# Performance work log

Measured on AMD Instinct MI355X. Metric: run time of the kernel, lower is better.

The kernel has to match this reference:

```python
import jax, jax.numpy as jnp
import numpy as np

D_MODEL = 1024
N_HEADS = 16
D_HEAD = 64
D_FF = 4096
WINDOW = 256
B, T = 2, 2048


def setup_inputs() -> dict:
    key = jax.random.key(0)
    ks = jax.random.split(key, 10)
    tot = N_HEADS * D_HEAD
    def w(k, shape):
        # approximate kaiming_normal_ fan_out init: std = sqrt(2/fan_out)
        fan_out = shape[0]
        return jax.random.normal(k, shape, jnp.float32) * np.sqrt(2.0 / fan_out)
    return {
        "x": jax.random.normal(ks[0], (B, T, D_MODEL), jnp.float32),
        "ln1_w": jnp.ones((D_MODEL,), jnp.float32),
        "qkv_w": w(ks[1], (3 * tot, D_MODEL)),
        "gate_w": w(ks[2], (tot, D_MODEL)),
        "out_w": w(ks[3], (D_MODEL, tot)),
        "ln2_w": jnp.ones((D_MODEL,), jnp.float32),
        "wg": w(ks[4], (D_FF, D_MODEL)),
        "wu": w(ks[5], (D_FF, D_MODEL)),
        "wo": w(ks[6], (D_MODEL, D_FF)),
    }


def _rmsnorm(x, w):
    return x * jax.lax.rsqrt(jnp.mean(x * x, axis=-1, keepdims=True) + 1e-6) * w


def _attention(x, qkv_w, gate_w, out_w):
    Bq, Tq, _ = x.shape
    tot = N_HEADS * D_HEAD
    qkv = x @ qkv_w.T  # [B,T,3*tot]
    q, k, v = jnp.split(qkv, 3, axis=-1)
    q = q.reshape(Bq, Tq, N_HEADS, D_HEAD).transpose(0, 2, 1, 3)
    k = k.reshape(Bq, Tq, N_HEADS, D_HEAD).transpose(0, 2, 1, 3)
    v = v.reshape(Bq, Tq, N_HEADS, D_HEAD).transpose(0, 2, 1, 3)
    scale = D_HEAD ** -0.5
    scores = jnp.einsum("bhqd,bhkd->bhqk", q, k) * scale
    pos = jnp.arange(Tq)
    dist = pos[:, None] - pos[None, :]
    allowed = (dist >= 0) & (dist < WINDOW)  # causal sliding window
    mask = jnp.where(allowed, 0.0, -jnp.inf).astype(scores.dtype)
    attn = jax.nn.softmax(scores + mask[None, None], axis=-1)
    out = jnp.einsum("bhqk,bhkd->bhqd", attn, v)
    out = out.transpose(0, 2, 1, 3).reshape(Bq, Tq, tot)
    gate = jax.nn.sigmoid(x @ gate_w.T)
    return (out * gate) @ out_w.T


def reference(x, ln1_w, qkv_w, gate_w, out_w, ln2_w, wg, wu, wo):
    x = x + _attention(_rmsnorm(x, ln1_w), qkv_w, gate_w, out_w)
    h = _rmsnorm(x, ln2_w)
    ffn = (jax.nn.silu(h @ wg.T) * (h @ wu.T)) @ wo.T
    return x + ffn
```

## Files before the change

### kernel.cpp

```cpp
#include <hip/hip_runtime.h>


#define DEV __device__ __forceinline__

using u16 = unsigned short;
typedef __attribute__((ext_vector_type(8))) short  short8;
typedef __attribute__((ext_vector_type(4))) float  floatx4;

DEV u16 f2bf(float f) {
  unsigned u = __builtin_bit_cast(unsigned, f);
  u += 0x7FFFu + ((u >> 16) & 1u);
  return (u16)(u >> 16);
}
DEV float bf2f(u16 h) {
  unsigned u = ((unsigned)h) << 16;
  return __builtin_bit_cast(float, u);
}
DEV floatx4 mfma16(short8 a, short8 b, floatx4 c) {
  return __builtin_amdgcn_mfma_f32_16x16x32_bf16(a, b, c, 0, 0, 0);
}
DEV void gload16(const u16* g, const char* lds_base_wave_uniform) {
  __builtin_amdgcn_global_load_lds(
      (const __attribute__((address_space(1))) void*)g,
      (__attribute__((address_space(3))) void*)lds_base_wave_uniform,
      16, 0, 0);
}
#define WAITVM(n) asm volatile("s_waitcnt vmcnt(" #n ")" ::: "memory")
DEV void blockbar() {
  asm volatile("" ::: "memory");
  __builtin_amdgcn_s_barrier();
  asm volatile("" ::: "memory");
}

__global__ __launch_bounds__(256) void cvt_all_k(
    const float* __restrict__ s0, const float* __restrict__ s1,
    const float* __restrict__ s2, const float* __restrict__ s3,
    const float* __restrict__ s4, const float* __restrict__ s5,
    u16* __restrict__ d0, u16* __restrict__ d1, u16* __restrict__ d2,
    u16* __restrict__ d3, u16* __restrict__ d4, u16* __restrict__ d5) {
  const int b = blockIdx.x;
  const float* in; u16* out; int base;
  if (b < 3072)       { in = s0; out = d0; base = 0; }
  else if (b < 4096)  { in = s1; out = d1; base = 3072; }
  else if (b < 5120)  { in = s2; out = d2; base = 4096; }
  else if (b < 9216)  { in = s3; out = d3; base = 5120; }
  else if (b < 13312) { in = s4; out = d4; base = 9216; }
  else                { in = s5; out = d5; base = 13312; }
  const size_t i = (size_t)(b - base) * 256 + threadIdx.x;
  const float4 v = ((const float4*)in)[i];
  ushort4 r;
  r.x = f2bf(v.x); r.y = f2bf(v.y); r.z = f2bf(v.z); r.w = f2bf(v.w);
  ((ushort4*)out)[i] = r;
}

__global__ __launch_bounds__(256) void rmsnorm_k(const float* __restrict__ x,
                                                 const float* __restrict__ wt,
                                                 u16* __restrict__ o) {
  __shared__ float red[4];
  const int row = blockIdx.x;
  const int tid = threadIdx.x;
  const float4 v = ((const float4*)(x + (size_t)row * 1024))[tid];
  float ss = v.x * v.x + v.y * v.y + v.z * v.z + v.w * v.w;
  ss += __shfl_xor(ss, 1, 64);
  ss += __shfl_xor(ss, 2, 64);
  ss += __shfl_xor(ss, 4, 64);
  ss += __shfl_xor(ss, 8, 64);
  ss += __shfl_xor(ss, 16, 64);
  ss += __shfl_xor(ss, 32, 64);
  if ((tid & 63) == 0) red[tid >> 6] = ss;
  __syncthreads();
  const float tot = red[0] + red[1] + red[2] + red[3];
  const float sc = rsqrtf(tot * (1.0f / 1024.0f) + 1e-6f);
  const float4 wv = ((const float4*)wt)[tid];
  ushort4 r;
  r.x = f2bf(v.x * sc * wv.x);
  r.y = f2bf(v.y * sc * wv.y);
  r.z = f2bf(v.z * sc * wv.z);
  r.w = f2bf(v.w * sc * wv.w);
  ((ushort4*)(o + (size_t)row * 1024))[tid] = r;
}

__global__ __launch_bounds__(256) void reduce4_k(const u16* __restrict__ part,
                                                 const float* __restrict__ x2,
                                                 float* __restrict__ out) {
  const size_t i = ((size_t)blockIdx.x * 256 + threadIdx.x) * 4;
  float4 r = *(const float4*)(x2 + i);
#pragma unroll
  for (int s = 0; s < 4; s++) {
    const ushort4 pv = *(const ushort4*)(part + (size_t)s * 4194304 + i);
    r.x += bf2f(pv.x); r.y += bf2f(pv.y); r.z += bf2f(pv.z); r.w += bf2f(pv.w);
  }
  *(float4*)(out + i) = r;
}

template <int CFG, int EPI>
__global__ __launch_bounds__(512, 2) void gemm8p(
    const u16* __restrict__ Ag, const u16* __restrict__ Bg, int N, int K,
    int ksz, u16* __restrict__ cb, float* __restrict__ cf,
    const u16* __restrict__ aux, const float* __restrict__ resid,
    u16* __restrict__ cb2) {
  constexpr int BM = (CFG == 0) ? 256 : 128;
  constexpr int WM = (CFG == 0) ? 128 : 64;
  constexpr int WN = (CFG == 0) ? 64 : 32;
  constexpr int NI = WM / 16;
  constexpr int NJ = WN / 16;
  constexpr int IH = (CFG == 0) ? NI / 2 : NI;
  constexpr int GB = BM * 64;
  constexpr int QI = (CFG == 0) ? 2 : 1;
  constexpr int BUFB = 4 * GB;
  __shared__ __align__(16) char lds[2 * BUFB];

  const int tid = threadIdx.x;
  const int w = tid >> 6, lane = tid & 63;
  const int wm = w >> 2, wn = w & 3;
  const int g = lane >> 4, r16 = lane & 15;
  const int gx = (g ^ ((r16 >> 1) & 3)) << 4;

  int bid = blockIdx.y * gridDim.x + blockIdx.x;
  const int cpx = (gridDim.x * gridDim.y) >> 3;
  bid = (bid & 7) * cpx + (bid >> 3);
  const int m0 = (bid / gridDim.x) * BM;
  const int n0 = (bid % gridDim.x) * BM;
  const int kbeg = blockIdx.z * ksz;

  floatx4 acc[NI][NJ];
#pragma unroll
  for (int i = 0; i < NI; i++)
#pragma unroll
    for (int j = 0; j < NJ; j++) acc[i][j] = (floatx4){0.f, 0.f, 0.f, 0.f};

  const int nt = ksz >> 6;

  const int kg_src = (lane & 3) ^ ((lane >> 3) & 3);
  auto stageG = [&](int G, int t) {
    if (t >= nt) return;
    const u16* Mat = (G < 2) ? Ag : Bg;
    const int b0 = (G < 2) ? m0 : n0;
    const int kc = kbeg + t * 64 + (G & 1) * 32 + kg_src * 8;
    const char* dst = lds + (t & 1) * BUFB + G * GB + w * 1024;
#pragma unroll
    for (int q = 0; q < QI; q++) {
      const int row = q * 128 + w * 16 + (lane >> 2);
      gload16(Mat + (size_t)(b0 + row) * K + kc, dst + q * 8192);
    }
  };

  auto rdA = [&](short8* af, int ks, int ihalf, const char* buf) {
#pragma unroll
    for (int i = 0; i < IH; i++) {
      const int arow = wm * WM + (ihalf * IH + i) * 16 + r16;
      af[i] = *(const short8*)(buf + ks * GB + arow * 64 + gx);
    }
  };
  auto rdB = [&](short8* bf_, int ks, const char* buf) {
#pragma unroll
    for (int j = 0; j < NJ; j++) {
      const int brow = wn * WN + j * 16 + r16;
      bf_[j] = *(const short8*)(buf + 2 * GB + ks * GB + brow * 64 + gx);
    }
  };
  auto mm = [&](short8* af, short8* bf_, int ihalf) {
    __builtin_amdgcn_s_setprio(1);
#pragma unroll
    for (int i = 0; i < IH; i++)
#pragma unroll
      for (int j = 0; j < NJ; j++)
        acc[ihalf * IH + i][j] = mfma16(af[i], bf_[j], acc[ihalf * IH + i][j]);
    __builtin_amdgcn_s_setprio(0);
  };

  stageG(0, 0); stageG(2, 0); stageG(1, 0); stageG(3, 0);

  for (int t = 0; t < nt; ++t) {
    const char* buf = lds + (t & 1) * BUFB;
    if constexpr (CFG == 0) {
      short8 af0[IH], af1[IH], bfv[NJ];
      WAITVM(4);
      blockbar();
      rdA(af0, 0, 0, buf); rdB(bfv, 0, buf);
      stageG(0, t + 1);
      rdA(af1, 0, 1, buf);
      mm(af0, bfv, 0);
      blockbar();
      stageG(2, t + 1);
      mm(af1, bfv, 1);
      if (t + 1 < nt) { WAITVM(4); } else { WAITVM(0); }
      blockbar();
      rdA(af0, 1, 0, buf); rdB(bfv, 1, buf);
      stageG(1, t + 1);
      rdA(af1, 1, 1, buf);
      mm(af0, bfv, 0);
      blockbar();
      stageG(3, t + 1);
      mm(af1, bfv, 1);
    } else {
      short8 af[IH], bfv[NJ];
      WAITVM(2);
      blockbar();
      rdA(af, 0, 0, buf); rdB(bfv, 0, buf);
      stageG(0, t + 1); stageG(2, t + 1);
      mm(af, bfv, 0);
      if (t + 1 < nt) { WAITVM(2); } else { WAITVM(0); }
      blockbar();
      rdA(af, 1, 0, buf); rdB(bfv, 1, buf);
      stageG(1, t + 1); stageG(3, t + 1);
      mm(af, bfv, 0);
    }
  }

#pragma unroll
  for (int i = 0; i < NI; i++) {
    const int row = m0 + wm * WM + i * 16 + g * 4;
#pragma unroll
    for (int j = 0; j < NJ; j++) {
      const int col = n0 + wn * WN + j * 16 + r16;
#pragma unroll
      for (int rr = 0; rr < 4; rr++) {
        const float v = acc[i][j][rr];
        if constexpr (EPI == 2) {
          cb[(size_t)(row + rr) * N + col] = f2bf(v / (1.0f + __expf(-v)));
        } else if constexpr (EPI == 3) {
          const size_t idx = (size_t)(row + rr) * N + col;
          cb[idx] = f2bf(v * bf2f(aux[idx]));
        } else if constexpr (EPI == 4) {
          const size_t idx = (size_t)(row + rr) * N + col;
          cf[idx] = v + resid[idx];
        } else if constexpr (EPI == 6) {
          if (col < 3072)
            cb[(size_t)(row + rr) * 3072 + col] = f2bf(v);
          else
            cb2[(size_t)(row + rr) * 1024 + (col - 3072)] =
                f2bf(1.0f / (1.0f + __expf(-v)));
        } else if constexpr (EPI == 7) {
          (cb + (size_t)blockIdx.z * 4194304)[(size_t)(row + rr) * N + col] =
              f2bf(v);
        }
      }
    }
  }
}

__global__ __launch_bounds__(256) void attn_win_kernel(
    const u16* __restrict__ qkv, const u16* __restrict__ gate,
    u16* __restrict__ out) {
  __shared__ __align__(16) u16 Kl[64][80];
  __shared__ __align__(16) u16 Vt[64][80];
  __shared__ __align__(16) u16 Pl[4][16][80];

  const int tid = threadIdx.x;
  const int w = tid >> 6, lane = tid & 63;
  const int g = lane >> 4, r16 = lane & 15;

  const int q0 = blockIdx.x * 64;
  const int h = blockIdx.y;
  const int b = blockIdx.z;
  const u16* qb_ = qkv + (size_t)b * 2048 * 3072;

  const int tq = q0 + w * 16 + r16;
  const u16* qptr = qb_ + (size_t)tq * 3072 + h * 64;
  const short8 aq0 = *(const short8*)(qptr + g * 8);
  const short8 aq1 = *(const short8*)(qptr + 32 + g * 8);

  floatx4 O[4] = {{0,0,0,0},{0,0,0,0},{0,0,0,0},{0,0,0,0}};
  float mrow[4] = {-1e30f, -1e30f, -1e30f, -1e30f};
  float lrow[4] = {0.f, 0.f, 0.f, 0.f};

  const int srow = tid >> 2;
  const int sq4 = tid & 3;
  const int qw = q0 + w * 16;

  for (int kt = q0 - 256; kt <= q0; kt += 64) {
    if (kt < 0) continue;
    {
      const u16* kb = qb_ + (size_t)(kt + srow) * 3072 + 1024 + h * 64 + sq4 * 16;
      const short8 kv0 = *(const short8*)kb;
      const short8 kv1 = *(const short8*)(kb + 8);
      *(short8*)&Kl[srow][sq4 * 16] = kv0;
      *(short8*)&Kl[srow][sq4 * 16 + 8] = kv1;
      const u16* vb = kb + 1024;
      const short8 vv0 = *(const short8*)vb;
      const short8 vv1 = *(const short8*)(vb + 8);
#pragma unroll
      for (int j = 0; j < 8; j++) Vt[sq4 * 16 + j][srow] = (u16)vv0[j];
#pragma unroll
      for (int j = 0; j < 8; j++) Vt[sq4 * 16 + 8 + j][srow] = (u16)vv1[j];
    }
    __syncthreads();

    const bool active = (qw + 15 >= kt) && (qw - kt < 319);
    if (active) {
      floatx4 S[4];
#pragma unroll
      for (int nf = 0; nf < 4; nf++) {
        const short8 bk0 = *(const short8*)&Kl[nf * 16 + r16][g * 8];
        const short8 bk1 = *(const short8*)&Kl[nf * 16 + r16][32 + g * 8];
        floatx4 a = {0.f, 0.f, 0.f, 0.f};
        a = mfma16(aq0, bk0, a);
        a = mfma16(aq1, bk1, a);
        S[nf] = a;
      }
      float pm[4][4];
      float nmax[4] = {-1e30f, -1e30f, -1e30f, -1e30f};
#pragma unroll
      for (int nf = 0; nf < 4; nf++) {
        const int key = kt + nf * 16 + r16;
#pragma unroll
        for (int rr = 0; rr < 4; rr++) {
          const int q = qw + g * 4 + rr;
          const int dist = q - key;
          const float s = (dist >= 0 && dist < 256) ? S[nf][rr] : -1e30f;
          pm[nf][rr] = s;
          nmax[rr] = fmaxf(nmax[rr], s);
        }
      }
#pragma unroll
      for (int rr = 0; rr < 4; rr++) {
        float v = nmax[rr];
        v = fmaxf(v, __shfl_xor(v, 1, 64));
        v = fmaxf(v, __shfl_xor(v, 2, 64));
        v = fmaxf(v, __shfl_xor(v, 4, 64));
        v = fmaxf(v, __shfl_xor(v, 8, 64));
        const float mnew = fmaxf(mrow[rr], v);
        const float alpha = __expf(0.125f * (mrow[rr] - mnew));
        mrow[rr] = mnew;
        lrow[rr] *= alpha;
#pragma unroll
        for (int n = 0; n < 4; n++) O[n][rr] *= alpha;
        float ls = 0.f;
#pragma unroll
        for (int nf = 0; nf < 4; nf++) {
          const float s = pm[nf][rr];
          const float pv = (s < -1e29f) ? 0.f : __expf(0.125f * (s - mnew));
          pm[nf][rr] = pv;
          ls += pv;
        }
        ls += __shfl_xor(ls, 1, 64);
        ls += __shfl_xor(ls, 2, 64);
        ls += __shfl_xor(ls, 4, 64);
        ls += __shfl_xor(ls, 8, 64);
        lrow[rr] += ls;
      }
#pragma unroll
      for (int nf = 0; nf < 4; nf++)
#pragma unroll
        for (int rr = 0; rr < 4; rr++)
          Pl[w][g * 4 + rr][nf * 16 + r16] = f2bf(pm[nf][rr]);
#pragma unroll
      for (int kf = 0; kf < 2; kf++) {
        const short8 pa = *(const short8*)&Pl[w][r16][kf * 32 + g * 8];
#pragma unroll
        for (int n = 0; n < 4; n++) {
          const short8 vb8 = *(const short8*)&Vt[n * 16 + r16][kf * 32 + g * 8];
          O[n] = mfma16(pa, vb8, O[n]);
        }
      }
    }
    __syncthreads();
  }

#pragma unroll
  for (int n = 0; n < 4; n++) {
#pragma unroll
    for (int rr = 0; rr < 4; rr++) {
      const int t = qw + g * 4 + rr;
      const size_t idx = ((size_t)(b * 2048 + t)) * 1024 + h * 64 + n * 16 + r16;
      const float gv = bf2f(gate[idx]);
      const float ov = (O[n][rr] / lrow[rr]) * gv;
      out[idx] = f2bf(ov);
    }
  }
}

extern "C" void kernel_launch(void* const* d_in, const int* in_sizes, int n_in,
                              void* d_out, int out_size, void* d_ws,
                              size_t ws_size, hipStream_t stream) {
  (void)in_sizes; (void)n_in; (void)out_size; (void)ws_size;
  const float* x     = (const float*)d_in[0];
  const float* ln1   = (const float*)d_in[1];
  const float* qkvw  = (const float*)d_in[2];
  const float* gatew = (const float*)d_in[3];
  const float* outw  = (const float*)d_in[4];
  const float* ln2   = (const float*)d_in[5];
  const float* wg    = (const float*)d_in[6];
  const float* wu    = (const float*)d_in[7];
  const float* wo    = (const float*)d_in[8];
  float* outp = (float*)d_out;

  u16* p = (u16*)d_ws;
  u16* qkvw_b  = p; p += 3 * 1024 * 1024;
  u16* gatew_b = p; p += 1024 * 1024;
  u16* outw_b  = p; p += 1024 * 1024;
  u16* wg_b    = p; p += 4 * 1024 * 1024;
  u16* wu_b    = p; p += 4 * 1024 * 1024;
  u16* wo_b    = p; p += 4 * 1024 * 1024;
  u16* xn      = p; p += 4096 * 1024;
  u16* qkvb    = p; p += (size_t)4096 * 3072;
  u16* gates   = p; p += 4096 * 1024;
  u16* a3      = p; p += 4096 * 1024;
  u16* hb      = p; p += 4096 * 1024;
  u16* gs      = p; p += (size_t)4096 * 4096;
  float* x2    = (float*)p;
  u16* parts   = xn;

  cvt_all_k<<<17408, 256, 0, stream>>>(qkvw, gatew, outw, wg, wu, wo,
                                       qkvw_b, gatew_b, outw_b, wg_b, wu_b, wo_b);

  rmsnorm_k<<<4096, 256, 0, stream>>>(x, ln1, xn);

  gemm8p<0, 6><<<dim3(16, 16), 512, 0, stream>>>(
      xn, qkvw_b, 4096, 1024, 1024, qkvb, nullptr, nullptr, nullptr, gates);

  attn_win_kernel<<<dim3(32, 16, 2), 256, 0, stream>>>(qkvb, gates, a3);

  gemm8p<1, 4><<<dim3(8, 32), 512, 0, stream>>>(
      a3, outw_b, 1024, 1024, 1024, nullptr, x2, nullptr, x, nullptr);

  rmsnorm_k<<<4096, 256, 0, stream>>>(x2, ln2, hb);

  gemm8p<0, 2><<<dim3(16, 16), 512, 0, stream>>>(
      hb, wg_b, 4096, 1024, 1024, gs, nullptr, nullptr, nullptr, nullptr);
  gemm8p<0, 3><<<dim3(16, 16), 512, 0, stream>>>(
      hb, wu_b, 4096, 1024, 1024, gs, nullptr, gs, nullptr, nullptr);

  gemm8p<0, 7><<<dim3(4, 16, 4), 512, 0, stream>>>(
      gs, wo_b, 1024, 4096, 1024, parts, nullptr, nullptr, nullptr, nullptr);
  reduce4_k<<<4096, 256, 0, stream>>>(parts, x2, outp);
}
```

Before: 360.5 us.

## Deepen GEMM global-to-LDS pipeline with half-tile prefetch two steps ahead

Restructures the bf16 MFMA GEMM main loop so that the K-half units of the shared-memory double buffer are refilled at finer granularity. The first-half A/B units for tile t+2 are issued as soon as tile t's first half has been consumed, and a prologue preloads ahead with explicit vmcnt thresholds. The LDS swizzle changes from XOR to an add-rotate pattern, and explicit lgkmcnt waits plus extra barriers are inserted around each MFMA batch. This is meant to hide global load latency better, at the cost of more block-wide barriers per iteration.

```diff
diff --git a/kernel.cpp b/kernel.cpp
--- a/kernel.cpp
+++ b/kernel.cpp
@@ -26,6 +26,7 @@
       16, 0, 0);
 }
 #define WAITVM(n) asm volatile("s_waitcnt vmcnt(" #n ")" ::: "memory")
+#define LGKM0    asm volatile("s_waitcnt lgkmcnt(0)" ::: "memory")
 DEV void blockbar() {
   asm volatile("" ::: "memory");
   __builtin_amdgcn_s_barrier();
@@ -104,17 +105,15 @@
   constexpr int WN = (CFG == 0) ? 64 : 32;
   constexpr int NI = WM / 16;
   constexpr int NJ = WN / 16;
-  constexpr int IH = (CFG == 0) ? NI / 2 : NI;
-  constexpr int GB = BM * 64;
+  constexpr int UB = BM * 64;
   constexpr int QI = (CFG == 0) ? 2 : 1;
-  constexpr int BUFB = 4 * GB;
-  __shared__ __align__(16) char lds[2 * BUFB];
+  __shared__ __align__(16) char lds[2 * 4 * UB];
 
   const int tid = threadIdx.x;
   const int w = tid >> 6, lane = tid & 63;
   const int wm = w >> 2, wn = w & 3;
   const int g = lane >> 4, r16 = lane & 15;
-  const int gx = (g ^ ((r16 >> 1) & 3)) << 4;
+  const int gxr = ((g + ((r16 >> 1) & 3)) & 3) << 4;
 
   int bid = blockIdx.y * gridDim.x + blockIdx.x;
   const int cpx = (gridDim.x * gridDim.y) >> 3;
@@ -131,80 +130,91 @@
 
   const int nt = ksz >> 6;
 
-  const int kg_src = (lane & 3) ^ ((lane >> 3) & 3);
-  auto stageG = [&](int G, int t) {
+  const int srow0 = w * 16 + (lane >> 2);
+  const int scol8 = (((lane & 3) - ((lane >> 3) & 3)) & 3) * 8;
+
+  auto stageG = [&](int U, int t) {
     if (t >= nt) return;
-    const u16* Mat = (G < 2) ? Ag : Bg;
-    const int b0 = (G < 2) ? m0 : n0;
-    const int kc = kbeg + t * 64 + (G & 1) * 32 + kg_src * 8;
-    const char* dst = lds + (t & 1) * BUFB + G * GB + w * 1024;
-#pragma unroll
-    for (int q = 0; q < QI; q++) {
-      const int row = q * 128 + w * 16 + (lane >> 2);
-      gload16(Mat + (size_t)(b0 + row) * K + kc, dst + q * 8192);
-    }
+    const u16* Mat = (U < 2) ? Ag : Bg;
+    const int b0 = (U < 2) ? m0 : n0;
+    const int kc = kbeg + t * 64 + (U & 1) * 32 + scol8;
+    const char* dst = lds + (t & 1) * (4 * UB) + U * UB + w * 1024;
+#pragma unroll
+    for (int q = 0; q < QI; q++)
+      gload16(Mat + (size_t)(b0 + srow0 + q * 128) * K + kc, dst + q * 8192);
   };
 
-  auto rdA = [&](short8* af, int ks, int ihalf, const char* buf) {
-#pragma unroll
-    for (int i = 0; i < IH; i++) {
-      const int arow = wm * WM + (ihalf * IH + i) * 16 + r16;
-      af[i] = *(const short8*)(buf + ks * GB + arow * 64 + gx);
+  auto rdA = [&](short8* af, int ks, int ih, const char* buf) {
+#pragma unroll
+    for (int i = 0; i < 4; i++) {
+      const int arow = wm * WM + (ih * 4 + i) * 16 + r16;
+      af[i] = *(const short8*)(buf + ks * UB + arow * 64 + gxr);
     }
   };
-  auto rdB = [&](short8* bf_, int ks, const char* buf) {
+  auto rdB = [&](short8* bv, int ks, const char* buf) {
 #pragma unroll
     for (int j = 0; j < NJ; j++) {
       const int brow = wn * WN + j * 16 + r16;
-      bf_[j] = *(const short8*)(buf + 2 * GB + ks * GB + brow * 64 + gx);
+      bv[j] = *(const short8*)(buf + (2 + ks) * UB + brow * 64 + gxr);
     }
   };
-  auto mm = [&](short8* af, short8* bf_, int ihalf) {
+  auto mm = [&](short8* af, short8* bv, int ih) {
     __builtin_amdgcn_s_setprio(1);
 #pragma unroll
-    for (int i = 0; i < IH; i++)
+    for (int i = 0; i < 4; i++)
 #pragma unroll
       for (int j = 0; j < NJ; j++)
-        acc[ihalf * IH + i][j] = mfma16(af[i], bf_[j], acc[ihalf * IH + i][j]);
+        acc[ih * 4 + i][j] = mfma16(af[i], bv[j], acc[ih * 4 + i][j]);
     __builtin_amdgcn_s_setprio(0);
   };
 
   stageG(0, 0); stageG(2, 0); stageG(1, 0); stageG(3, 0);
+  stageG(0, 1); stageG(2, 1);
+  if constexpr (CFG == 0) { WAITVM(8); } else { WAITVM(4); }
+  blockbar();
 
   for (int t = 0; t < nt; ++t) {
-    const char* buf = lds + (t & 1) * BUFB;
+    const char* buf = lds + (t & 1) * (4 * UB);
     if constexpr (CFG == 0) {
-      short8 af0[IH], af1[IH], bfv[NJ];
-      WAITVM(4);
-      blockbar();
-      rdA(af0, 0, 0, buf); rdB(bfv, 0, buf);
-      stageG(0, t + 1);
-      rdA(af1, 0, 1, buf);
-      mm(af0, bfv, 0);
-      blockbar();
-      stageG(2, t + 1);
-      mm(af1, bfv, 1);
+      short8 a0[4], a1[4], bv[NJ];
+      rdA(a0, 0, 0, buf); rdB(bv, 0, buf);
+      stageG(1, t + 1);
+      blockbar(); LGKM0;
+      mm(a0, bv, 0);
+      blockbar();
+      rdA(a1, 0, 1, buf);
+      stageG(3, t + 1);
+      blockbar(); LGKM0;
+      mm(a1, bv, 1);
+      if (t + 1 < nt) { WAITVM(8); } else { WAITVM(0); }
+      blockbar();
+      rdA(a0, 1, 0, buf); rdB(bv, 1, buf);
+      stageG(0, t + 2);
+      blockbar(); LGKM0;
+      mm(a0, bv, 0);
+      blockbar();
+      rdA(a1, 1, 1, buf);
+      stageG(2, t + 2);
+      blockbar(); LGKM0;
+      mm(a1, bv, 1);
+      if (t + 2 < nt) { WAITVM(8); }
+      else if (t + 1 < nt) { WAITVM(4); }
+      blockbar();
+    } else {
+      short8 a0[4], bv[NJ];
+      rdA(a0, 0, 0, buf); rdB(bv, 0, buf);
+      stageG(1, t + 1); stageG(3, t + 1);
+      blockbar(); LGKM0;
+      mm(a0, bv, 0);
       if (t + 1 < nt) { WAITVM(4); } else { WAITVM(0); }
       blockbar();
-      rdA(af0, 1, 0, buf); rdB(bfv, 1, buf);
-      stageG(1, t + 1);
-      rdA(af1, 1, 1, buf);
-      mm(af0, bfv, 0);
-      blockbar();
-      stageG(3, t + 1);
-      mm(af1, bfv, 1);
-    } else {
-      short8 af[IH], bfv[NJ];
-      WAITVM(2);
-      blockbar();
-      rdA(af, 0, 0, buf); rdB(bfv, 0, buf);
-      stageG(0, t + 1); stageG(2, t + 1);
-      mm(af, bfv, 0);
-      if (t + 1 < nt) { WAITVM(2); } else { WAITVM(0); }
-      blockbar();
-      rdA(af, 1, 0, buf); rdB(bfv, 1, buf);
-      stageG(1, t + 1); stageG(3, t + 1);
-      mm(af, bfv, 0);
+      rdA(a0, 1, 0, buf); rdB(bv, 1, buf);
+      stageG(0, t + 2); stageG(2, t + 2);
+      blockbar(); LGKM0;
+      mm(a0, bv, 0);
+      if (t + 2 < nt) { WAITVM(4); }
+      else if (t + 1 < nt) { WAITVM(2); }
+      blockbar();
     }
   }
 
```

After: 362.5 us. About the same (+0.6%).
